# Kernel optimization log

Measured on AMD Instinct MI355X. Metric: run time of the kernel, lower is better.

The kernel has to match this reference:

```python
import jax, jax.numpy as jnp
import numpy as np

B, N, D, H = 2, 2048, 1024, 16
DH = D // H  # head dim = 64


def setup_inputs() -> dict:
    key = jax.random.key(0)
    k1, k2, k3 = jax.random.split(key, 3)
    x = jax.random.normal(k1, (B, N, D), dtype=jnp.float32)
    # per-head Linear(D, 3*DH): stacked weights (H, D, 3*DH), biases (H, 3*DH)
    W_qkv = jax.random.normal(k2, (H, D, 3 * DH), dtype=jnp.float32) * 0.02
    b_qkv = jnp.zeros((H, 3 * DH), dtype=jnp.float32)
    W_proj = jax.random.normal(k3, (D, D), dtype=jnp.float32) * 0.02
    b_proj = jnp.zeros((D,), dtype=jnp.float32)
    return {"x": x, "W_qkv": W_qkv, "b_qkv": b_qkv, "W_proj": W_proj, "b_proj": b_proj}


def reference(x, W_qkv, b_qkv, W_proj, b_proj):
    b, n, d = x.shape
    h = W_qkv.shape[0]
    dh = W_qkv.shape[2] // 3
    # all heads' kqv projections at once: (B, H, N, 3*DH)
    qkv = jnp.einsum('bnd,hde->bhne', x, W_qkv) + b_qkv[None, :, None, :]
    # original chunks in order k, q, v
    k, q, v = jnp.split(qkv, 3, axis=-1)  # each (B, H, N, DH)
    # scores[b,h,n,m] = q_n . k_m / sqrt(dh)
    scores = jnp.einsum('bhnd,bhmd->bhnm', q, k) / jnp.sqrt(jnp.asarray(dh, x.dtype))
    causal = jnp.tril(jnp.ones((n, n), dtype=bool))
    scores = jnp.where(causal[None, None, :, :], scores, -jnp.inf)
    A = jax.nn.softmax(scores, axis=-1)
    out = jnp.einsum('bhnm,bhmd->bhnd', A, v)
    # concat heads (head-major order matches the torch cat over head list)
    out = out.transpose(0, 2, 1, 3).reshape(b, n, h * dh)
    return out @ W_proj + b_proj
```

## Files before the change

kernel.cpp:

```cpp
#include <hip/hip_runtime.h>
#include <hip/hip_bf16.h>

typedef __hip_bfloat16 HBF;
typedef __bf16 bf16x8 __attribute__((ext_vector_type(8)));
typedef __bf16 bf16x4 __attribute__((ext_vector_type(4)));
typedef float f32x4 __attribute__((ext_vector_type(4)));
typedef float float4v __attribute__((ext_vector_type(4)));

__device__ __forceinline__ float toF(float x) { return x; }
__device__ __forceinline__ float toF(HBF x) { return __bfloat162float(x); }

#define MFMA16(a, b, c) __builtin_amdgcn_mfma_f32_16x16x32_bf16((a), (b), (c), 0, 0, 0)
#define EXP2F(x) __builtin_amdgcn_exp2f(x)
#define QSCALE 0.18033688011112042f
#define MEMFENCE asm volatile("" ::: "memory")

__device__ __forceinline__ void gload_lds16(const HBF* g, HBF* l) {
  __builtin_amdgcn_global_load_lds((const __attribute__((address_space(1))) void*)g,
                                   (__attribute__((address_space(3))) void*)l, 16, 0, 0);
}

__global__ void prep_k(const float* __restrict__ x, HBF* __restrict__ xb,
                       const float* __restrict__ Wqkv, HBF* __restrict__ wqkv_t,
                       const float* __restrict__ Wproj, HBF* __restrict__ wproj_t) {
  const int bid = blockIdx.x, tid = threadIdx.x;
  if (bid < 4096) {
    int i = bid * 256 + tid;
    float4v a = reinterpret_cast<const float4v*>(x)[i];
    HBF o[4] = {__float2bfloat16(a.x), __float2bfloat16(a.y),
                __float2bfloat16(a.z), __float2bfloat16(a.w)};
    *reinterpret_cast<ulonglong1*>(&xb[i * 4]) = *reinterpret_cast<ulonglong1*>(o);
    return;
  }
  __shared__ float tile[32][33];
  const float* in;
  HBF* out;
  int R, C, gx, gy;
  size_t base;
  if (bid < 7168) {
    int t = bid - 4096;
    int gz = t / 192, rem = t % 192;
    gy = rem / 6; gx = rem % 6;
    R = 1024; C = 192;
    base = (size_t)gz * R * C;
    in = Wqkv; out = wqkv_t;
  } else {
    int t = bid - 7168;
    gy = t / 32; gx = t % 32;
    R = 1024; C = 1024;
    base = 0;
    in = Wproj; out = wproj_t;
  }
  int r0 = gy * 32, c0 = gx * 32;
  int tx = tid & 31, ty = tid >> 5;
#pragma unroll
  for (int i = ty; i < 32; i += 8)
    tile[i][tx] = in[base + (size_t)(r0 + i) * C + c0 + tx];
  __syncthreads();
#pragma unroll
  for (int i = ty; i < 32; i += 8)
    out[base + (size_t)(c0 + i) * R + r0 + tx] = __float2bfloat16(tile[tx][i]);
}

__launch_bounds__(512, 1)
__global__ void gemm_qkv_8ph(const HBF* __restrict__ A, const HBF* __restrict__ Bt,
                             const float* __restrict__ bias,
                             HBF* __restrict__ Kout, HBF* __restrict__ Qout,
                             HBF* __restrict__ Vtout) {
  __shared__ __align__(16) HBF As[2][16384];
  __shared__ __align__(16) HBF Bs[2][12288];
  const int tid = threadIdx.x, lane = tid & 63, w = tid >> 6;
  const int lo = lane & 15, g4 = lane >> 4;
  const int wr = w >> 2, wc = w & 3;
  const int s = ((int)blockIdx.x & 7) * 32 + ((int)blockIdx.x >> 3);
  const int bx = s & 15, by = s >> 4;
  const int m0 = by * 256, n0 = bx * 192;
  const int NT = 16;

  f32x4 acc[8][3];
#pragma unroll
  for (int i = 0; i < 8; i++)
#pragma unroll
    for (int j = 0; j < 3; j++) acc[i][j] = (f32x4){0.f, 0.f, 0.f, 0.f};
  bf16x8 af[8][2], bfr[3][2];

  const int rl0 = w * 8 + (lane >> 3);
  const int rl1 = 64 + rl0;
  const int kc0 = (lane & 7) ^ (rl0 & 7);
  const int kc1 = (lane & 7) ^ (rl1 & 7);

  auto stageA = [&](int kt, int hf) {
    HBF* base = &As[kt & 1][hf * 8192];
    const int r0g = m0 + hf * 128;
    gload_lds16(A + (size_t)(r0g + rl0) * 1024 + kt * 64 + kc0 * 8, base + w * 512);
    gload_lds16(A + (size_t)(r0g + rl1) * 1024 + kt * 64 + kc1 * 8, base + 4096 + w * 512);
  };
  auto stageB = [&](int kt, int g) {
    gload_lds16(Bt + (size_t)(n0 + g * 64 + rl0) * 1024 + kt * 64 + kc0 * 8,
                &Bs[kt & 1][g * 4096] + w * 512);
  };
  auto ldA = [&](int bb, int mt, int ks) -> bf16x8 {
    int row = wr * 128 + mt * 16 + lo;
    return *reinterpret_cast<const bf16x8*>(&As[bb][row * 64 + ((ks * 32 + g4 * 8) ^ ((row & 7) * 8))]);
  };
  auto ldB = [&](int bb, int nt, int ks) -> bf16x8 {
    int row = wc * 48 + nt * 16 + lo;
    return *reinterpret_cast<const bf16x8*>(&Bs[bb][row * 64 + ((ks * 32 + g4 * 8) ^ ((row & 7) * 8))]);
  };

  stageA(0, 0); stageA(0, 1); stageB(0, 0); stageB(0, 1); stageB(0, 2);
  stageA(1, 0); stageA(1, 1);
  asm volatile("s_waitcnt vmcnt(4)" ::: "memory");
  __builtin_amdgcn_s_barrier();
  MEMFENCE;

  for (int t = 0; t < NT; ++t) {
    const int bb = t & 1;
#pragma unroll
    for (int mt = 0; mt < 4; ++mt) { af[mt][0] = ldA(bb, mt, 0); af[mt][1] = ldA(bb, mt, 1); }
#pragma unroll
    for (int nt = 0; nt < 2; ++nt) { bfr[nt][0] = ldB(bb, nt, 0); bfr[nt][1] = ldB(bb, nt, 1); }
    if (t + 1 < NT) stageB(t + 1, 0);
    MEMFENCE; __builtin_amdgcn_s_barrier(); MEMFENCE;
    __builtin_amdgcn_s_setprio(1);
#pragma unroll
    for (int mt = 0; mt < 4; ++mt)
#pragma unroll
      for (int nt = 0; nt < 2; ++nt)
#pragma unroll
        for (int ks = 0; ks < 2; ++ks) acc[mt][nt] = MFMA16(af[mt][ks], bfr[nt][ks], acc[mt][nt]);
    __builtin_amdgcn_s_setprio(0);
    MEMFENCE; __builtin_amdgcn_s_barrier(); MEMFENCE;
#pragma unroll
    for (int mt = 4; mt < 8; ++mt) { af[mt][0] = ldA(bb, mt, 0); af[mt][1] = ldA(bb, mt, 1); }
    if (t + 1 < NT) { stageB(t + 1, 1); stageB(t + 1, 2); }
    MEMFENCE; __builtin_amdgcn_s_barrier(); MEMFENCE;
    __builtin_amdgcn_s_setprio(1);
#pragma unroll
    for (int mt = 4; mt < 8; ++mt)
#pragma unroll
      for (int nt = 0; nt < 2; ++nt)
#pragma unroll
        for (int ks = 0; ks < 2; ++ks) acc[mt][nt] = MFMA16(af[mt][ks], bfr[nt][ks], acc[mt][nt]);
    __builtin_amdgcn_s_setprio(0);
    MEMFENCE; __builtin_amdgcn_s_barrier(); MEMFENCE;
    bfr[2][0] = ldB(bb, 2, 0); bfr[2][1] = ldB(bb, 2, 1);
    if (t + 2 < NT) stageA(t + 2, 0);
    MEMFENCE; __builtin_amdgcn_s_barrier(); MEMFENCE;
    __builtin_amdgcn_s_setprio(1);
#pragma unroll
    for (int mt = 0; mt < 4; ++mt)
#pragma unroll
      for (int ks = 0; ks < 2; ++ks) acc[mt][2] = MFMA16(af[mt][ks], bfr[2][ks], acc[mt][2]);
    __builtin_amdgcn_s_setprio(0);
    MEMFENCE; __builtin_amdgcn_s_barrier(); MEMFENCE;
    if (t + 2 < NT) stageA(t + 2, 1);
    MEMFENCE; __builtin_amdgcn_s_barrier(); MEMFENCE;
    __builtin_amdgcn_s_setprio(1);
#pragma unroll
    for (int mt = 4; mt < 8; ++mt)
#pragma unroll
      for (int ks = 0; ks < 2; ++ks) acc[mt][2] = MFMA16(af[mt][ks], bfr[2][ks], acc[mt][2]);
    __builtin_amdgcn_s_setprio(0);
    asm volatile("s_waitcnt vmcnt(4)" ::: "memory");
    __builtin_amdgcn_s_barrier();
    MEMFENCE;
  }

#pragma unroll
  for (int mt = 0; mt < 8; ++mt) {
    int mrow = m0 + wr * 128 + mt * 16 + g4 * 4;
#pragma unroll
    for (int nt = 0; nt < 3; ++nt) {
      int e = wc * 48 + nt * 16 + lo;
      float bv = bias[bx * 192 + e];
#pragma unroll
      for (int r = 0; r < 4; ++r) {
        int mm = mrow + r;
        int b = mm >> 11, n = mm & 2047;
        float v = acc[mt][nt][r] + bv;
        size_t bh64 = (size_t)(b * 16 + bx);
        if (e < 64)       Kout[(bh64 * 2048 + n) * 64 + e] = __float2bfloat16(v);
        else if (e < 128) Qout[(bh64 * 2048 + n) * 64 + e - 64] = __float2bfloat16(v * QSCALE);
        else              Vtout[(bh64 * 64 + (e - 128)) * 2048 + n] = __float2bfloat16(v);
      }
    }
  }
}

__launch_bounds__(256)
__global__ void gemm_proj_k(const HBF* __restrict__ A, const HBF* __restrict__ Bt,
                            int M, int N, int K, const float* __restrict__ bias,
                            float* __restrict__ Cout) {
  __shared__ __align__(16) HBF As[128 * 64];
  __shared__ __align__(16) HBF Bs[128 * 64];
  const int tid = threadIdx.x;
  const int lane = tid & 63;
  const int w = tid >> 6;
  const int lo = lane & 15, g4 = lane >> 4;
  const int m0 = blockIdx.y * 128, n0 = blockIdx.x * 128;
  const int wr = w >> 1, wc = w & 1;

  const f32x4 zero = {0.f, 0.f, 0.f, 0.f};
  f32x4 acc[4][4];
#pragma unroll
  for (int i = 0; i < 4; i++)
#pragma unroll
    for (int j = 0; j < 4; j++) acc[i][j] = zero;

  for (int k0 = 0; k0 < K; k0 += 64) {
#pragma unroll
    for (int c = 0; c < 4; ++c) {
      int chunk = c * 256 + tid;
      int row = chunk >> 3, kc = (chunk & 7) * 8;
      HBF* ldsA = As + (size_t)(c * 256 + w * 64) * 8;
      HBF* ldsB = Bs + (size_t)(c * 256 + w * 64) * 8;
      gload_lds16(A + (size_t)(m0 + row) * K + k0 + kc, ldsA);
      gload_lds16(Bt + (size_t)(n0 + row) * K + k0 + kc, ldsB);
    }
    __syncthreads();
#pragma unroll
    for (int kk = 0; kk < 2; ++kk) {
      bf16x8 af[4], bfr[4];
#pragma unroll
      for (int i = 0; i < 4; i++)
        af[i] = *reinterpret_cast<const bf16x8*>(As + (size_t)(wr * 64 + i * 16 + lo) * 64 + kk * 32 + g4 * 8);
#pragma unroll
      for (int j = 0; j < 4; j++)
        bfr[j] = *reinterpret_cast<const bf16x8*>(Bs + (size_t)(wc * 64 + j * 16 + lo) * 64 + kk * 32 + g4 * 8);
#pragma unroll
      for (int i = 0; i < 4; i++)
#pragma unroll
        for (int j = 0; j < 4; j++) acc[i][j] = MFMA16(af[i], bfr[j], acc[i][j]);
    }
    __syncthreads();
  }

#pragma unroll
  for (int i = 0; i < 4; i++) {
    int mrow = m0 + wr * 64 + i * 16 + g4 * 4;
#pragma unroll
    for (int j = 0; j < 4; j++) {
      int col = n0 + wc * 64 + j * 16 + lo;
      float bv = bias[col];
#pragma unroll
      for (int r = 0; r < 4; r++)
        Cout[(size_t)(mrow + r) * N + col] = acc[i][j][r] + bv;
    }
  }
}

__launch_bounds__(256, 2)
__global__ void attn_fwd_k(const HBF* __restrict__ Qb, const HBF* __restrict__ Kb,
                           const HBF* __restrict__ Vt, HBF* __restrict__ Ob) {
  __shared__ __align__(16) HBF Ks[2][2][4096];
  __shared__ __align__(16) HBF Vs[2][2][4096];
  __shared__ __align__(16) HBF pLds[4][2048];
  const int tid = threadIdx.x;
  const int lane = tid & 63;
  const int w = tid >> 6;
  const int lo = lane & 15, g4 = lane >> 4;

  const int lin = blockIdx.x;
  const int xcd = lin & 7, c = lin >> 3;
  const int bh = xcd * 4 + (c & 3);
  const int j = 31 - (c >> 2);
  const int b = bh >> 4, h = bh & 15;
  const int qrow0 = j * 64 + w * 16;
  const int nkv = (j + 2) >> 1;

  const HBF* Qp = Qb + (size_t)bh * 2048 * 64;
  const HBF* Kp = Kb + (size_t)bh * 2048 * 64;
  const HBF* Vp = Vt + (size_t)bh * 64 * 2048;

  bf16x8 qf[2];
#pragma unroll
  for (int ds = 0; ds < 2; ds++)
    qf[ds] = *reinterpret_cast<const bf16x8*>(Qp + (size_t)(qrow0 + lo) * 64 + ds * 32 + g4 * 8);

  const f32x4 zero = {0.f, 0.f, 0.f, 0.f};
  f32x4 o[4];
  float m = -1e30f, l = 0.f;
#pragma unroll
  for (int j4 = 0; j4 < 4; j4++) o[j4] = zero;

  const int srow = (lane >> 3) & 7;
  const int sch = lane & 7;
  const int psw = (lo & 7) << 4;

  auto stage = [&](int kv0, int sb) {
#pragma unroll
    for (int sub = 0; sub < 2; sub++)
#pragma unroll
      for (int cc = 0; cc < 2; cc++) {
        int seg = w * 2 + cc;
        int row = seg * 8 + srow;
        gload_lds16(Kp + (size_t)(kv0 + sub * 64 + row) * 64 + ((sch ^ (row & 7)) * 8),
                    &Ks[sb][sub][seg * 512]);
        gload_lds16(Vp + (size_t)row * 2048 + kv0 + sub * 64 + ((sch ^ (row & 7)) * 8),
                    &Vs[sb][sub][seg * 512]);
      }
  };

  stage(0, 0);
  __syncthreads();

  for (int t = 0; t < nkv; ++t) {
    const int kv0 = t * 128;
    const int sb = t & 1;
    if (t + 1 < nkv) stage(kv0 + 128, sb ^ 1);

    f32x4 st[2][4];
#pragma unroll
    for (int sub = 0; sub < 2; sub++)
#pragma unroll
      for (int kt = 0; kt < 4; kt++) {
        int krow = kt * 16 + lo;
        bf16x8 kf0 = *reinterpret_cast<const bf16x8*>(&Ks[sb][sub][krow * 64 + ((g4 ^ (krow & 7)) * 8)]);
        bf16x8 kf1 = *reinterpret_cast<const bf16x8*>(&Ks[sb][sub][krow * 64 + (((4 + g4) ^ (krow & 7)) * 8)]);
        f32x4 z = zero;
        z = MFMA16(kf0, qf[0], z);
        z = MFMA16(kf1, qf[1], z);
        st[sub][kt] = z;
      }

    const int q = qrow0 + lo;
    float pmax = -1e30f;
    if (t == nkv - 1) {
#pragma unroll
      for (int sub = 0; sub < 2; sub++)
#pragma unroll
        for (int kt = 0; kt < 4; kt++)
#pragma unroll
          for (int r = 0; r < 4; r++) {
            int key = kv0 + sub * 64 + kt * 16 + g4 * 4 + r;
            float v = (key <= q) ? st[sub][kt][r] : -1e30f;
            st[sub][kt][r] = v;
            pmax = fmaxf(pmax, v);
          }
    } else {
#pragma unroll
      for (int sub = 0; sub < 2; sub++)
#pragma unroll
        for (int kt = 0; kt < 4; kt++)
#pragma unroll
          for (int r = 0; r < 4; r++) pmax = fmaxf(pmax, st[sub][kt][r]);
    }
    pmax = fmaxf(pmax, __shfl_xor(pmax, 16));
    pmax = fmaxf(pmax, __shfl_xor(pmax, 32));
    if (__any(pmax > m + 11.5f)) {
      float mn = fmaxf(m, pmax);
      float al = EXP2F(m - mn);
      m = mn;
      l *= al;
      float alr[4];
#pragma unroll
      for (int r = 0; r < 4; r++) alr[r] = __shfl(al, g4 * 4 + r);
#pragma unroll
      for (int j4 = 0; j4 < 4; j4++)
#pragma unroll
        for (int r = 0; r < 4; r++) o[j4][r] *= alr[r];
    }
#pragma unroll
    for (int sub = 0; sub < 2; sub++)
#pragma unroll
      for (int kt = 0; kt < 4; kt++)
#pragma unroll
        for (int r = 0; r < 4; r++) {
          float p = EXP2F(st[sub][kt][r] - m);
          st[sub][kt][r] = p;
          l += p;
        }
#pragma unroll
    for (int sub = 0; sub < 2; sub++)
#pragma unroll
      for (int kt = 0; kt < 4; kt++) {
        bf16x4 pk;
#pragma unroll
        for (int r = 0; r < 4; r++) pk[r] = (__bf16)st[sub][kt][r];
        *reinterpret_cast<bf16x4*>(
            &pLds[w][lo * 128 + (((sub * 128 + kt * 32 + g4 * 8) ^ psw) >> 1)]) = pk;
      }
    asm volatile("s_waitcnt lgkmcnt(0)" ::: "memory");
    __builtin_amdgcn_sched_barrier(0);

    bf16x8 pa[4];
#pragma unroll
    for (int ks = 0; ks < 4; ks++)
      pa[ks] = *reinterpret_cast<const bf16x8*>(
          &pLds[w][lo * 128 + (((ks * 64 + g4 * 16) ^ psw) >> 1)]);
#pragma unroll
    for (int j4 = 0; j4 < 4; j4++) {
      int vrow = j4 * 16 + lo;
#pragma unroll
      for (int ks = 0; ks < 4; ks++) {
        bf16x8 vb = *reinterpret_cast<const bf16x8*>(
            &Vs[sb][ks >> 1][vrow * 64 + ((((ks & 1) * 4 + g4) ^ (vrow & 7)) * 8)]);
        o[j4] = MFMA16(pa[ks], vb, o[j4]);
      }
    }
    __syncthreads();
  }

  l += __shfl_xor(l, 16);
  l += __shfl_xor(l, 32);
  float linv = 1.f / l;
  float lr[4];
#pragma unroll
  for (int r = 0; r < 4; r++) lr[r] = __shfl(linv, g4 * 4 + r);
#pragma unroll
  for (int j4 = 0; j4 < 4; j4++)
#pragma unroll
    for (int r = 0; r < 4; r++) {
      int q = qrow0 + g4 * 4 + r;
      Ob[(size_t)(b * 2048 + q) * 1024 + h * 64 + j4 * 16 + lo] =
          __float2bfloat16(o[j4][r] * lr[r]);
    }
}

extern "C" void kernel_launch(void* const* d_in, const int* in_sizes, int n_in,
                              void* d_out, int out_size, void* d_ws, size_t ws_size,
                              hipStream_t stream) {
  const float* x      = (const float*)d_in[0];
  const float* W_qkv  = (const float*)d_in[1];
  const float* b_qkv  = (const float*)d_in[2];
  const float* W_proj = (const float*)d_in[3];
  const float* b_proj = (const float*)d_in[4];
  float* out = (float*)d_out;

  const int B = 2, N = 2048, D = 1024, H = 16, DH = 64;
  const int M = B * N;

  char* ws = (char*)d_ws;
  HBF* xb      = (HBF*)ws; ws += (size_t)M * D * 2;
  HBF* wqkv_t  = (HBF*)ws; ws += (size_t)H * 3 * DH * D * 2;
  HBF* wproj_t = (HBF*)ws; ws += (size_t)D * D * 2;
  HBF* Qb      = (HBF*)ws; ws += (size_t)B * H * N * DH * 2;
  HBF* Kb      = (HBF*)ws; ws += (size_t)B * H * N * DH * 2;
  HBF* Vt      = (HBF*)ws; ws += (size_t)B * H * DH * N * 2;
  HBF* Ob      = (HBF*)ws; ws += (size_t)M * D * 2;

  prep_k<<<8192, 256, 0, stream>>>(x, xb, W_qkv, wqkv_t, W_proj, wproj_t);
  gemm_qkv_8ph<<<256, 512, 0, stream>>>(xb, wqkv_t, b_qkv, Kb, Qb, Vt);
  attn_fwd_k<<<1024, 256, 0, stream>>>(Qb, Kb, Vt, Ob);
  gemm_proj_k<<<dim3(D / 128, M / 128), 256, 0, stream>>>(Ob, wproj_t, M, D, D, b_proj, out);
}
```

Baseline: 111.8 us.

## Halve QKV GEMM M-tile to 128 and double grid to 512 blocks

The QKV projection GEMM tile shrinks from 256x192 to 128x192, which halves the A shared-memory buffer and the per-wave accumulators. The grid doubles to 512 blocks and launch bounds now allow several blocks per CU. The eight-phase pipeline is collapsed into four phases with matching vmcnt waits. The aim is to fill all 256 CUs and get better latency hiding, at the cost of less reuse of each loaded B tile.

```diff
diff --git a/kernel.cpp b/kernel.cpp
--- a/kernel.cpp
+++ b/kernel.cpp
@@ -62,45 +62,44 @@
     out[base + (size_t)(c0 + i) * R + r0 + tx] = __float2bfloat16(tile[tx][i]);
 }
 
-__launch_bounds__(512, 1)
+__launch_bounds__(512, 4)
 __global__ void gemm_qkv_8ph(const HBF* __restrict__ A, const HBF* __restrict__ Bt,
                              const float* __restrict__ bias,
                              HBF* __restrict__ Kout, HBF* __restrict__ Qout,
                              HBF* __restrict__ Vtout) {
-  __shared__ __align__(16) HBF As[2][16384];
+  __shared__ __align__(16) HBF As[2][8192];
   __shared__ __align__(16) HBF Bs[2][12288];
   const int tid = threadIdx.x, lane = tid & 63, w = tid >> 6;
   const int lo = lane & 15, g4 = lane >> 4;
   const int wr = w >> 2, wc = w & 3;
-  const int s = ((int)blockIdx.x & 7) * 32 + ((int)blockIdx.x >> 3);
+  const int s = ((int)blockIdx.x & 7) * 64 + ((int)blockIdx.x >> 3);
   const int bx = s & 15, by = s >> 4;
-  const int m0 = by * 256, n0 = bx * 192;
+  const int m0 = by * 128, n0 = bx * 192;
   const int NT = 16;
 
-  f32x4 acc[8][3];
-#pragma unroll
-  for (int i = 0; i < 8; i++)
+  f32x4 acc[4][3];
+#pragma unroll
+  for (int i = 0; i < 4; i++)
 #pragma unroll
     for (int j = 0; j < 3; j++) acc[i][j] = (f32x4){0.f, 0.f, 0.f, 0.f};
-  bf16x8 af[8][2], bfr[3][2];
+  bf16x8 af[4][2], bfr[3][2];
 
   const int rl0 = w * 8 + (lane >> 3);
   const int rl1 = 64 + rl0;
   const int kc0 = (lane & 7) ^ (rl0 & 7);
   const int kc1 = (lane & 7) ^ (rl1 & 7);
 
-  auto stageA = [&](int kt, int hf) {
-    HBF* base = &As[kt & 1][hf * 8192];
-    const int r0g = m0 + hf * 128;
-    gload_lds16(A + (size_t)(r0g + rl0) * 1024 + kt * 64 + kc0 * 8, base + w * 512);
-    gload_lds16(A + (size_t)(r0g + rl1) * 1024 + kt * 64 + kc1 * 8, base + 4096 + w * 512);
+  auto stageA = [&](int kt) {
+    HBF* base = &As[kt & 1][0];
+    gload_lds16(A + (size_t)(m0 + rl0) * 1024 + kt * 64 + kc0 * 8, base + w * 512);
+    gload_lds16(A + (size_t)(m0 + rl1) * 1024 + kt * 64 + kc1 * 8, base + 4096 + w * 512);
   };
   auto stageB = [&](int kt, int g) {
     gload_lds16(Bt + (size_t)(n0 + g * 64 + rl0) * 1024 + kt * 64 + kc0 * 8,
                 &Bs[kt & 1][g * 4096] + w * 512);
   };
   auto ldA = [&](int bb, int mt, int ks) -> bf16x8 {
-    int row = wr * 128 + mt * 16 + lo;
+    int row = wr * 64 + mt * 16 + lo;
     return *reinterpret_cast<const bf16x8*>(&As[bb][row * 64 + ((ks * 32 + g4 * 8) ^ ((row & 7) * 8))]);
   };
   auto ldB = [&](int bb, int nt, int ks) -> bf16x8 {
@@ -108,9 +107,9 @@
     return *reinterpret_cast<const bf16x8*>(&Bs[bb][row * 64 + ((ks * 32 + g4 * 8) ^ ((row & 7) * 8))]);
   };
 
-  stageA(0, 0); stageA(0, 1); stageB(0, 0); stageB(0, 1); stageB(0, 2);
-  stageA(1, 0); stageA(1, 1);
-  asm volatile("s_waitcnt vmcnt(4)" ::: "memory");
+  stageA(0); stageB(0, 0); stageB(0, 1); stageB(0, 2);
+  stageA(1);
+  asm volatile("s_waitcnt vmcnt(2)" ::: "memory");
   __builtin_amdgcn_s_barrier();
   MEMFENCE;
 
@@ -131,45 +130,28 @@
         for (int ks = 0; ks < 2; ++ks) acc[mt][nt] = MFMA16(af[mt][ks], bfr[nt][ks], acc[mt][nt]);
     __builtin_amdgcn_s_setprio(0);
     MEMFENCE; __builtin_amdgcn_s_barrier(); MEMFENCE;
-#pragma unroll
-    for (int mt = 4; mt < 8; ++mt) { af[mt][0] = ldA(bb, mt, 0); af[mt][1] = ldA(bb, mt, 1); }
+    bfr[2][0] = ldB(bb, 2, 0); bfr[2][1] = ldB(bb, 2, 1);
     if (t + 1 < NT) { stageB(t + 1, 1); stageB(t + 1, 2); }
+    if (t + 2 < NT) stageA(t + 2);
     MEMFENCE; __builtin_amdgcn_s_barrier(); MEMFENCE;
     __builtin_amdgcn_s_setprio(1);
 #pragma unroll
-    for (int mt = 4; mt < 8; ++mt)
-#pragma unroll
-      for (int nt = 0; nt < 2; ++nt)
-#pragma unroll
-        for (int ks = 0; ks < 2; ++ks) acc[mt][nt] = MFMA16(af[mt][ks], bfr[nt][ks], acc[mt][nt]);
-    __builtin_amdgcn_s_setprio(0);
-    MEMFENCE; __builtin_amdgcn_s_barrier(); MEMFENCE;
-    bfr[2][0] = ldB(bb, 2, 0); bfr[2][1] = ldB(bb, 2, 1);
-    if (t + 2 < NT) stageA(t + 2, 0);
-    MEMFENCE; __builtin_amdgcn_s_barrier(); MEMFENCE;
-    __builtin_amdgcn_s_setprio(1);
-#pragma unroll
     for (int mt = 0; mt < 4; ++mt)
 #pragma unroll
       for (int ks = 0; ks < 2; ++ks) acc[mt][2] = MFMA16(af[mt][ks], bfr[2][ks], acc[mt][2]);
     __builtin_amdgcn_s_setprio(0);
-    MEMFENCE; __builtin_amdgcn_s_barrier(); MEMFENCE;
-    if (t + 2 < NT) stageA(t + 2, 1);
-    MEMFENCE; __builtin_amdgcn_s_barrier(); MEMFENCE;
-    __builtin_amdgcn_s_setprio(1);
-#pragma unroll
-    for (int mt = 4; mt < 8; ++mt)
-#pragma unroll
-      for (int ks = 0; ks < 2; ++ks) acc[mt][2] = MFMA16(af[mt][ks], bfr[2][ks], acc[mt][2]);
-    __builtin_amdgcn_s_setprio(0);
-    asm volatile("s_waitcnt vmcnt(4)" ::: "memory");
+    if (t + 2 < NT) {
+      asm volatile("s_waitcnt vmcnt(2)" ::: "memory");
+    } else {
+      asm volatile("s_waitcnt vmcnt(0)" ::: "memory");
+    }
     __builtin_amdgcn_s_barrier();
     MEMFENCE;
   }
 
 #pragma unroll
-  for (int mt = 0; mt < 8; ++mt) {
-    int mrow = m0 + wr * 128 + mt * 16 + g4 * 4;
+  for (int mt = 0; mt < 4; ++mt) {
+    int mrow = m0 + wr * 64 + mt * 16 + g4 * 4;
 #pragma unroll
     for (int nt = 0; nt < 3; ++nt) {
       int e = wc * 48 + nt * 16 + lo;
@@ -441,7 +423,7 @@
   HBF* Ob      = (HBF*)ws; ws += (size_t)M * D * 2;
 
   prep_k<<<8192, 256, 0, stream>>>(x, xb, W_qkv, wqkv_t, W_proj, wproj_t);
-  gemm_qkv_8ph<<<256, 512, 0, stream>>>(xb, wqkv_t, b_qkv, Kb, Qb, Vt);
+  gemm_qkv_8ph<<<512, 512, 0, stream>>>(xb, wqkv_t, b_qkv, Kb, Qb, Vt);
   attn_fwd_k<<<1024, 256, 0, stream>>>(Qb, Kb, Vt, Ob);
   gemm_proj_k<<<dim3(D / 128, M / 128), 256, 0, stream>>>(Ob, wproj_t, M, D, D, b_proj, out);
 }
```

Result: faster. 104.9 us (-6.1%).
